# Kernel tuning notes

Hardware: AMD Instinct MI355X
Metric: run time of the kernel (lower is better)

Reference implementation:

```python
import jax, jax.numpy as jnp
import numpy as np

D_MODEL = 1024
N_HEADS = 16
D_HEAD = 64  # = d_model // num_heads = d_inner
LN_EPS = 1e-5


def setup_inputs() -> dict:
    key = jax.random.key(0)
    ks = jax.random.split(key, 8)
    B, CUR, PREV = 2, 1024, 1024
    T = CUR + PREV
    s = 0.02
    return {
        "x": jax.random.normal(ks[0], (B, CUR, D_MODEL), jnp.float32),
        "pos_emb": jax.random.normal(ks[1], (T, D_MODEL), jnp.float32),
        "u": jax.random.normal(ks[2], (N_HEADS, D_HEAD), jnp.float32),
        "v": jax.random.normal(ks[3], (N_HEADS, D_HEAD), jnp.float32),
        "tgt_mask": jnp.ones((B, CUR, T, 1), jnp.bool_),
        "mem": jax.random.normal(ks[4], (B, PREV, D_MODEL), jnp.float32),
        "Wq": jax.random.normal(ks[5], (D_MODEL, D_MODEL), jnp.float32) * s,
        "Wkv": jax.random.normal(ks[6], (2 * D_MODEL, D_MODEL), jnp.float32) * s,
        "Wfc": jax.random.normal(ks[7], (D_MODEL, D_MODEL), jnp.float32) * s,
        "bfc": jnp.zeros((D_MODEL,), jnp.float32),
        "gamma": jnp.ones((D_MODEL,), jnp.float32),
        "beta": jnp.zeros((D_MODEL,), jnp.float32),
    }


def _rel_shift(x):
    # Faithful port of the torch _rel_shift: pad along the query axis (dim=1),
    # reinterpret the contiguous buffer as (I+1, B, J, H), drop first row, reshape back.
    B, I, J, H = x.shape
    zero_pad = jnp.zeros((B, 1, J, H), x.dtype)
    x_padded = jnp.concatenate([zero_pad, x], axis=1).reshape(I + 1, B, J, H)
    return x_padded[1:].reshape(B, I, J, H)


def reference(x, pos_emb, u, v, tgt_mask, mem, Wq, Wkv, Wfc, bfc, gamma, beta):
    B, CUR, _ = x.shape
    h = jnp.concatenate([mem, x], axis=1)          # (B, T, d_model)
    T = h.shape[1]
    q = (x @ Wq.T).reshape(B, CUR, N_HEADS, D_HEAD)
    kv = h @ Wkv.T                                  # (B, T, 2*d_model)
    k, vv = jnp.split(kv, 2, axis=-1)
    k = k.reshape(B, T, N_HEADS, D_HEAD)
    vv = vv.reshape(B, T, N_HEADS, D_HEAD)

    content_attn = jnp.einsum('bihd,bjhd->bijh', q + u, k)
    pe = pos_emb.reshape(T, N_HEADS, D_HEAD)
    pos_attn = _rel_shift(jnp.einsum('bihd,jhd->bijh', q + v, pe))

    attn = content_attn + pos_attn                  # (B, I, J, H)
    attn = jnp.where(tgt_mask == 0, -jnp.inf, attn)  # mask BEFORE scaling (as original)
    attn = attn / (D_HEAD ** 0.5)
    attn = jax.nn.softmax(attn, axis=1)             # NOTE: original softmaxes over dim=1 (query axis)

    weighted = jnp.einsum('bijh,bjhd->bihd', attn, vv).reshape(B, CUR, -1)
    y = x + weighted @ Wfc.T + bfc                  # residual + fc (post-norm path)
    mu = jnp.mean(y, axis=-1, keepdims=True)
    var = jnp.var(y, axis=-1, keepdims=True)
    return (y - mu) / jnp.sqrt(var + LN_EPS) * gamma + beta
```

## Files before the change

### kernel.cpp

```cpp
#include <hip/hip_runtime.h>

#define DM   1024
#define CUR  1024
#define TT   2048

typedef float  f32x4  __attribute__((ext_vector_type(4)));
typedef __bf16 bf16_t;
typedef __bf16 bf16x8 __attribute__((ext_vector_type(8)));
typedef __bf16 bf16x4 __attribute__((ext_vector_type(4)));
typedef short  s16x4  __attribute__((ext_vector_type(4)));

#define SCALE_A 0.18033688f

static __device__ __forceinline__ float exp2fast(float x) { return __builtin_amdgcn_exp2f(x); }

static __device__ __forceinline__ f32x4 mfma32(bf16x8 a, bf16x8 b, f32x4 c) {
  return __builtin_amdgcn_mfma_f32_16x16x32_bf16(a, b, c, 0, 0, 0);
}
static __device__ __forceinline__ f32x4 mfma16(bf16x4 a, bf16x4 b, f32x4 c) {
  return __builtin_amdgcn_mfma_f32_16x16x16bf16_1k(
      __builtin_bit_cast(s16x4, a), __builtin_bit_cast(s16x4, b), c, 0, 0, 0);
}
static __device__ __forceinline__ void gl_lds16(const bf16_t* g, bf16_t* l) {
  __builtin_amdgcn_global_load_lds(
      (const __attribute__((address_space(1))) void*)g,
      (__attribute__((address_space(3))) void*)l, 16, 0, 0);
}

__global__ __launch_bounds__(256) void prep_kernel(const float* __restrict__ Wq,
                                                   const float* __restrict__ Wkv,
                                                   const float* __restrict__ Wfc,
                                                   const float* __restrict__ mem,
                                                   const float* __restrict__ x,
                                                   const float* __restrict__ pos,
                                                   bf16_t* __restrict__ wqb,
                                                   bf16_t* __restrict__ wkvb,
                                                   bf16_t* __restrict__ wfcb,
                                                   bf16_t* __restrict__ hb,
                                                   bf16_t* __restrict__ Bs) {
  int t = blockIdx.x * 256 + threadIdx.x;
  if (t < (1 << 20)) {
    const float* src; bf16_t* dst; int off;
    if (t < 262144)      { src = Wq;  dst = wqb;  off = t; }
    else if (t < 786432) { src = Wkv; dst = wkvb; off = t - 262144; }
    else                 { src = Wfc; dst = wfcb; off = t - 786432; }
    f32x4 v = *(const f32x4*)(src + (size_t)off * 4);
    bf16x4 o;
    o[0] = (bf16_t)v[0]; o[1] = (bf16_t)v[1]; o[2] = (bf16_t)v[2]; o[3] = (bf16_t)v[3];
    *(bf16x4*)(dst + (size_t)off * 4) = o;
  } else if (t < (2 << 20)) {
    int th = t - (1 << 20);
    int idx = th << 2;
    int b   = idx >> 21;
    int rem = idx & ((1 << 21) - 1);
    int tt  = rem >> 10;
    int c   = rem & 1023;
    const float* s = (tt < 1024)
        ? (mem + ((size_t)b * 1024 + tt) * DM + c)
        : (x   + ((size_t)b * 1024 + (tt - 1024)) * DM + c);
    f32x4 v = *(const f32x4*)s;
    bf16x4 o;
    o[0] = (bf16_t)v[0]; o[1] = (bf16_t)v[1]; o[2] = (bf16_t)v[2]; o[3] = (bf16_t)v[3];
    *(bf16x4*)(hb + idx) = o;
  } else {
    int tp = t - (2 << 20);
    int d4 = (tp & 15) << 2;
    int j  = (tp >> 4) & 2047;
    int bh = tp >> 15;
    int h  = bh & 15;
    f32x4 v = *(const f32x4*)(pos + (size_t)j * DM + h * 64 + d4);
    bf16x4 o;
    o[0] = (bf16_t)v[0]; o[1] = (bf16_t)v[1]; o[2] = (bf16_t)v[2]; o[3] = (bf16_t)v[3];
    *(bf16x4*)(Bs + ((size_t)bh * TT + j) * 128 + 64 + d4) = o;
  }
}

template<int WM>
__device__ __forceinline__ void gemm_core(const bf16_t* __restrict__ A,
                                          const bf16_t* __restrict__ B,
                                          int r0, int c0,
                                          bf16_t* At, bf16_t* Bt,
                                          f32x4 (&acc)[WM][4]) {
  const int ASZ = WM * 1024;
  const int BSZ = 4096;
  const int tid = threadIdx.x, w = tid >> 6, l = tid & 63;
  const int lm = l & 15, q = l >> 4;
  const int wrow = w >> 1, wcol = w & 1;
  const int gg  = (l & 3) ^ ((l >> 3) & 3);
  const int rsw = (lm >> 1) & 3;
  const bf16_t* gA = A + (size_t)(r0 + w * (WM / 2) * 16 + (l >> 2)) * 1024 + gg * 8;
  const bf16_t* gB = B + (size_t)(c0 + w * 32 + (l >> 2)) * 1024 + gg * 8;
  bf16_t* lA = At + w * (WM / 2) * 512;
  bf16_t* lB = Bt + w * 1024;
  const bf16_t* fA = At + (wrow * WM * 16 + lm) * 32;
  const bf16_t* fB = Bt + (wcol * 64 + lm) * 32;
#pragma unroll
  for (int t2 = 0; t2 < WM / 2; ++t2) gl_lds16(gA + (size_t)t2 * 16384, lA + t2 * 512);
#pragma unroll
  for (int t2 = 0; t2 < 2; ++t2)      gl_lds16(gB + (size_t)t2 * 16384, lB + t2 * 512);
  __syncthreads();
  int p = 0;
  for (int k0 = 0; k0 < 1024; k0 += 32) {
    int pn = p ^ 1;
    if (k0 < 992) {
#pragma unroll
      for (int t2 = 0; t2 < WM / 2; ++t2)
        gl_lds16(gA + (size_t)t2 * 16384 + k0 + 32, lA + pn * ASZ + t2 * 512);
#pragma unroll
      for (int t2 = 0; t2 < 2; ++t2)
        gl_lds16(gB + (size_t)t2 * 16384 + k0 + 32, lB + pn * BSZ + t2 * 512);
    }
    bf16x8 af[WM], bfm[4];
#pragma unroll
    for (int it = 0; it < WM; ++it)
      af[it] = *(const bf16x8*)(fA + p * ASZ + it * 512 + ((q ^ rsw) << 3));
#pragma unroll
    for (int jt = 0; jt < 4; ++jt)
      bfm[jt] = *(const bf16x8*)(fB + p * BSZ + jt * 512 + ((q ^ rsw) << 3));
#pragma unroll
    for (int it = 0; it < WM; ++it)
#pragma unroll
      for (int jt = 0; jt < 4; ++jt)
        acc[it][jt] = mfma32(af[it], bfm[jt], acc[it][jt]);
    __syncthreads();
    p = pn;
  }
}

__global__ __launch_bounds__(256) void k1_q(const bf16_t* __restrict__ hb,
                                            const bf16_t* __restrict__ Wqb,
                                            const float* __restrict__ u,
                                            const float* __restrict__ v,
                                            bf16_t* __restrict__ As) {
  __shared__ union { struct { bf16_t At[4096]; bf16_t Bt[8192]; } m; float Tt[4][272]; } sm;
  int blk = blockIdx.x;
  int r0 = (blk >> 3) * 64, c0 = (blk & 7) * 128;
  int b = r0 >> 10;
  const bf16_t* Axv = hb + ((size_t)(b + 1) << 20);
  f32x4 acc[2][4] = {};
  gemm_core<2>(Axv, Wqb, r0, c0, sm.m.At, sm.m.Bt, acc);
  const int tid = threadIdx.x, w = tid >> 6, l = tid & 63;
  const int lm = l & 15, q = l >> 4;
  const int wrow = w >> 1, wcol = w & 1;
  float* Tw = sm.Tt[w];
  int h = (c0 + wcol * 64) >> 6;
#pragma unroll
  for (int it = 0; it < 2; ++it) {
#pragma unroll
    for (int jt = 0; jt < 4; ++jt) {
#pragma unroll
      for (int r = 0; r < 4; ++r) Tw[(q * 4 + r) * 17 + lm] = acc[it][jt][r];
      __builtin_amdgcn_wave_barrier();
      int row = r0 + wrow * 32 + it * 16 + lm;
      int ii = row & 1023;
      int cbase = c0 + wcol * 64 + jt * 16 + q * 4;
      int d0 = cbase & 63;
      f32x4 u4 = *(const f32x4*)(u + cbase);
      f32x4 v4 = *(const f32x4*)(v + cbase);
      f32x4 tv;
#pragma unroll
      for (int e = 0; e < 4; ++e) tv[e] = Tw[lm * 17 + q * 4 + e];
      bf16x4 oc, op;
#pragma unroll
      for (int e = 0; e < 4; ++e) {
        oc[e] = (bf16_t)((tv[e] + u4[e]) * SCALE_A);
        op[e] = (bf16_t)((tv[e] + v4[e]) * SCALE_A);
      }
      *(bf16x4*)(As + (((size_t)(b * 16 + h)) * CUR + ii) * 128 + d0) = oc;
      if (b == 0) {
        if (ii >= 1)
          *(bf16x4*)(As + (((size_t)h) * CUR + (ii - 1)) * 128 + 64 + d0) = op;
        if (ii == 1023) {
          bf16x4 z = {};
          *(bf16x4*)(As + (((size_t)h) * CUR + 1023) * 128 + 64 + d0) = z;
        }
      } else {
        *(bf16x4*)(As + (((size_t)(16 + h)) * CUR + ii) * 128 + 64 + d0) = op;
      }
      __builtin_amdgcn_wave_barrier();
    }
  }
}

__global__ __launch_bounds__(256) void k2_kv(const bf16_t* __restrict__ hb,
                                             const bf16_t* __restrict__ Wkvb,
                                             bf16_t* __restrict__ Bs,
                                             bf16_t* __restrict__ vvT) {
  __shared__ union { struct { bf16_t At[8192]; bf16_t Bt[8192]; } m; float Tt[4][272]; } sm;
  int blk = blockIdx.x;
  int xcd = blk & 7, t = blk >> 3;
  int r0 = (t & 31) * 128;
  int c0 = (xcd * 2 + (t >> 5)) * 128;
  f32x4 acc[4][4] = {};
  gemm_core<4>(hb, Wkvb, r0, c0, sm.m.At, sm.m.Bt, acc);
  const int tid = threadIdx.x, w = tid >> 6, l = tid & 63;
  const int lm = l & 15, q = l >> 4;
  const int wrow = w >> 1, wcol = w & 1;
  int b = r0 >> 11;
  if (c0 < 1024) {
    float* Tw = sm.Tt[w];
    int h = (c0 + wcol * 64) >> 6;
#pragma unroll
    for (int it = 0; it < 4; ++it) {
#pragma unroll
      for (int jt = 0; jt < 4; ++jt) {
#pragma unroll
        for (int r = 0; r < 4; ++r) Tw[(q * 4 + r) * 17 + lm] = acc[it][jt][r];
        __builtin_amdgcn_wave_barrier();
        int j = (r0 + wrow * 64 + it * 16 + lm) & 2047;
        int d0 = jt * 16 + q * 4;
        bf16x4 o;
#pragma unroll
        for (int e = 0; e < 4; ++e) o[e] = (bf16_t)Tw[lm * 17 + q * 4 + e];
        *(bf16x4*)(Bs + (((size_t)(b * 16 + h)) * TT + j) * 128 + d0) = o;
        __builtin_amdgcn_wave_barrier();
      }
    }
  } else {
#pragma unroll
    for (int it = 0; it < 4; ++it) {
#pragma unroll
      for (int jt = 0; jt < 4; ++jt) {
        int c2 = c0 + wcol * 64 + jt * 16 + lm - 1024;
        int h = c2 >> 6, d = c2 & 63;
        int j = (r0 + wrow * 64 + it * 16 + q * 4) & 2047;
        bf16x4 o;
#pragma unroll
        for (int r = 0; r < 4; ++r) o[r] = (bf16_t)acc[it][jt][r];
        *(bf16x4*)(vvT + (((size_t)(b * 16 + h)) * 64 + d) * TT + j) = o;
      }
    }
  }
}

__global__ __launch_bounds__(256) void k3_stats(const bf16_t* __restrict__ As,
                                                const bf16_t* __restrict__ Bs,
                                                float* __restrict__ Lp) {
  __shared__ bf16_t At[2 * 8192];
  const int tid = threadIdx.x, w = tid >> 6, l = tid & 63;
  const int lm = l & 15, q = l >> 4;
  const int gg  = (l & 3) ^ ((l >> 3) & 3);
  const int rsw = (lm >> 1) & 3;
  int blk = blockIdx.x;
  int xcd = blk & 7, t = blk >> 3;
  int jblk = t & 7, ich = (t >> 3) & 3, bh = xcd * 4 + (t >> 5);
  int j0 = jblk * 256 + w * 64;
  const bf16_t* bsrow = Bs + ((size_t)bh * TT + j0 + lm) * 128 + q * 8;
  bf16x8 bfr[4][4];
#pragma unroll
  for (int js = 0; js < 4; ++js)
#pragma unroll
    for (int kt = 0; kt < 4; ++kt)
      bfr[js][kt] = *(const bf16x8*)(bsrow + js * 2048 + kt * 32);
  const bf16_t* abase = As + (size_t)bh * CUR * 128 +
                        (size_t)(ich * 256 + (l >> 2)) * 128 + w * 32 + gg * 8;
  bf16_t* lA = At + w * 2048;
  const bf16_t* fA = At + lm * 32;
  float lacc[4] = {0.f, 0.f, 0.f, 0.f};
#pragma unroll
  for (int t2 = 0; t2 < 4; ++t2)
    gl_lds16(abase + (size_t)t2 * 16 * 128, lA + t2 * 512);
  __syncthreads();
  int p = 0;
  for (int ib = 0; ib < 4; ++ib) {
    int pn = p ^ 1;
    if (ib < 3) {
#pragma unroll
      for (int t2 = 0; t2 < 4; ++t2)
        gl_lds16(abase + (size_t)((ib + 1) * 64 + t2 * 16) * 128, lA + pn * 8192 + t2 * 512);
    }
#pragma unroll
    for (int isub = 0; isub < 4; ++isub) {
      bf16x8 af[4];
#pragma unroll
      for (int kt = 0; kt < 4; ++kt)
        af[kt] = *(const bf16x8*)(fA + p * 8192 + kt * 2048 + isub * 512 + ((q ^ rsw) << 3));
      f32x4 s[4] = {};
#pragma unroll
      for (int js = 0; js < 4; ++js)
#pragma unroll
        for (int kt = 0; kt < 4; ++kt)
          s[js] = mfma32(af[kt], bfr[js][kt], s[js]);
#pragma unroll
      for (int js = 0; js < 4; ++js)
        lacc[js] += (exp2fast(s[js][0]) + exp2fast(s[js][1])) +
                    (exp2fast(s[js][2]) + exp2fast(s[js][3]));
    }
    __syncthreads();
    p = pn;
  }
#pragma unroll
  for (int js = 0; js < 4; ++js) {
#pragma unroll
    for (int off = 16; off <= 32; off <<= 1)
      lacc[js] += __shfl_xor(lacc[js], off, 64);
  }
  if (l < 16) {
    float* lp = Lp + (size_t)ich * 65536 + (size_t)bh * TT + j0;
#pragma unroll
    for (int js = 0; js < 4; ++js) lp[js * 16 + l] = lacc[js];
  }
}

__global__ __launch_bounds__(256) void vscale(const float* __restrict__ Lp,
                                              bf16_t* __restrict__ vvT) {
  int bh = blockIdx.x >> 3, jc = blockIdx.x & 7;
  int tid = threadIdx.x;
  int jj = jc * 256 + (tid & 63) * 4;
  int dg = tid >> 6;
  const float* lp = Lp + (size_t)bh * TT + jj;
  f32x4 a0 = *(const f32x4*)lp;
  f32x4 a1 = *(const f32x4*)(lp + 65536);
  f32x4 a2 = *(const f32x4*)(lp + 131072);
  f32x4 a3 = *(const f32x4*)(lp + 196608);
  f32x4 rl;
#pragma unroll
  for (int e = 0; e < 4; ++e)
    rl[e] = __builtin_amdgcn_rcpf((a0[e] + a1[e]) + (a2[e] + a3[e]));
  bf16_t* vb = vvT + ((size_t)bh * 64 + dg * 16) * TT + jj;
#pragma unroll
  for (int dd = 0; dd < 16; ++dd) {
    bf16x4 vv = *(const bf16x4*)(vb + (size_t)dd * TT);
    bf16x4 o;
#pragma unroll
    for (int e = 0; e < 4; ++e) o[e] = (bf16_t)((float)vv[e] * rl[e]);
    *(bf16x4*)(vb + (size_t)dd * TT) = o;
  }
}

__global__ __launch_bounds__(256, 2) void k4_attnv(const bf16_t* __restrict__ As,
                                                   const bf16_t* __restrict__ Bs,
                                                   const bf16_t* __restrict__ vvT,
                                                   bf16_t* __restrict__ Pp) {
  __shared__ union {
    struct { bf16_t Bt[2 * 8192]; bf16_t Vt[2 * 4096]; } m;
    float Tt[4][1088];
  } sm;
  int blk = blockIdx.x;
  int xcd = blk & 7, tb = blk >> 3;
  int iblk = tb & 3, pl = tb >> 2;
  int bh = xcd * 4 + (pl >> 3), jch = pl & 7;
  int b = bh >> 4, h = bh & 15;
  int i0 = iblk * 256;
  int jbase = jch * 256;
  const int tid = threadIdx.x, w = tid >> 6, l = tid & 63;
  const int lm = l & 15, q = l >> 4;
  const int gg  = (l & 3) ^ ((l >> 3) & 3);
  const int rsw = (lm >> 1) & 3;
  const bf16_t* ar = As + (size_t)bh * CUR * 128 + (size_t)(i0 + w * 64 + lm) * 128 + q * 8;
  bf16x8 bi[4][4];
#pragma unroll
  for (int is = 0; is < 4; ++is)
#pragma unroll
    for (int kt = 0; kt < 4; ++kt)
      bi[is][kt] = *(const bf16x8*)(ar + is * 2048 + kt * 32);
  const bf16_t* bbase = Bs + ((size_t)bh * TT + jbase) * 128 + (size_t)(l >> 2) * 128 + w * 32 + gg * 8;
  int inst0 = w * 2, inst1 = w * 2 + 1;
  const bf16_t* vsrc0 = vvT + ((size_t)bh * 64 + (inst0 & 3) * 16 + (l >> 2)) * TT + jbase +
                        (inst0 >> 2) * 32 + gg * 8;
  const bf16_t* vsrc1 = vvT + ((size_t)bh * 64 + (inst1 & 3) * 16 + (l >> 2)) * TT + jbase +
                        (inst1 >> 2) * 32 + gg * 8;
  bf16_t* vdst0 = sm.m.Vt + (inst0 >> 2) * 2048 + (inst0 & 3) * 512;
  bf16_t* vdst1 = sm.m.Vt + (inst1 >> 2) * 2048 + (inst1 & 3) * 512;
  bf16_t* lB = sm.m.Bt + w * 2048;
  f32x4 acc[4][4] = {};
#pragma unroll
  for (int t2 = 0; t2 < 4; ++t2)
    gl_lds16(bbase + (size_t)t2 * 16 * 128, lB + t2 * 512);
  gl_lds16(vsrc0, vdst0);
  gl_lds16(vsrc1, vdst1);
  __syncthreads();
  int p = 0;
  for (int jb = 0; jb < 4; ++jb) {
    int pn = p ^ 1;
    if (jb < 3) {
      const bf16_t* bs2 = bbase + (size_t)(jb + 1) * 64 * 128;
#pragma unroll
      for (int t2 = 0; t2 < 4; ++t2)
        gl_lds16(bs2 + (size_t)t2 * 16 * 128, lB + pn * 8192 + t2 * 512);
      gl_lds16(vsrc0 + (jb + 1) * 64, vdst0 + pn * 4096);
      gl_lds16(vsrc1 + (jb + 1) * 64, vdst1 + pn * 4096);
    }
    const bf16_t* fB = sm.m.Bt + p * 8192 + lm * 32;
    const bf16_t* vf = sm.m.Vt + p * 4096 + lm * 32;
#pragma unroll
    for (int js = 0; js < 4; ++js) {
      bf16x8 af[4];
#pragma unroll
      for (int kt = 0; kt < 4; ++kt)
        af[kt] = *(const bf16x8*)(fB + kt * 2048 + js * 512 + ((q ^ rsw) << 3));
      f32x4 s[4] = {};
#pragma unroll
      for (int is = 0; is < 4; ++is)
#pragma unroll
        for (int kt = 0; kt < 4; ++kt)
          s[is] = mfma32(af[kt], bi[is][kt], s[is]);
      bf16x4 pp[4];
#pragma unroll
      for (int is = 0; is < 4; ++is)
#pragma unroll
        for (int e = 0; e < 4; ++e)
          pp[is][e] = (bf16_t)exp2fast(s[is][e]);
      int vg = ((js & 1) << 1) | (q >> 1);
      const bf16_t* vfa = vf + (js >> 1) * 2048 + ((vg ^ rsw) << 3) + ((q & 1) << 2);
#pragma unroll
      for (int dt = 0; dt < 4; ++dt) {
        bf16x4 a2 = *(const bf16x4*)(vfa + dt * 512);
#pragma unroll
        for (int is = 0; is < 4; ++is)
          acc[is][dt] = mfma16(a2, pp[is], acc[is][dt]);
      }
    }
    __syncthreads();
    p = pn;
  }
  float* Tw = sm.Tt[w];
  bf16_t* pout = Pp + ((size_t)jch << 21);
  int ir = l >> 2, dc = (l & 3) * 16;
#pragma unroll
  for (int is = 0; is < 4; ++is) {
#pragma unroll
    for (int dt = 0; dt < 4; ++dt) {
      f32x4 a = acc[is][dt];
#pragma unroll
      for (int r = 0; r < 4; ++r) Tw[(dt * 16 + q * 4 + r) * 17 + lm] = a[r];
    }
    __builtin_amdgcn_wave_barrier();
    int i = i0 + w * 64 + is * 16 + ir;
    bf16_t* orow = pout + ((size_t)(b * CUR + i)) * DM + h * 64 + dc;
#pragma unroll
    for (int e4 = 0; e4 < 4; ++e4) {
      bf16x4 o;
#pragma unroll
      for (int e = 0; e < 4; ++e) o[e] = (bf16_t)Tw[(dc + e4 * 4 + e) * 17 + ir];
      *(bf16x4*)(orow + e4 * 4) = o;
    }
    __builtin_amdgcn_wave_barrier();
  }
}

__global__ __launch_bounds__(256) void k4_reduce(const bf16_t* __restrict__ P,
                                                 bf16_t* __restrict__ wbuf) {
  int t = blockIdx.x * 256 + threadIdx.x;
  float s[4] = {0.f, 0.f, 0.f, 0.f};
#pragma unroll
  for (int c = 0; c < 8; ++c) {
    bf16x4 v = *(const bf16x4*)(P + ((size_t)c << 21) + (size_t)t * 4);
#pragma unroll
    for (int e = 0; e < 4; ++e) s[e] += (float)v[e];
  }
  bf16x4 o;
#pragma unroll
  for (int e = 0; e < 4; ++e) o[e] = (bf16_t)s[e];
  *(bf16x4*)(wbuf + (size_t)t * 4) = o;
}

__global__ __launch_bounds__(256) void k5_fc(const bf16_t* __restrict__ wb,
                                             const bf16_t* __restrict__ Wfcb,
                                             const float* __restrict__ x,
                                             const float* __restrict__ bfc,
                                             float* __restrict__ y) {
  __shared__ union { struct { bf16_t At[4096]; bf16_t Bt[8192]; } m; float Tt[4][272]; } sm;
  int blk = blockIdx.x;
  int r0 = (blk >> 3) * 64, c0 = (blk & 7) * 128;
  f32x4 acc[2][4] = {};
  gemm_core<2>(wb, Wfcb, r0, c0, sm.m.At, sm.m.Bt, acc);
  const int tid = threadIdx.x, w = tid >> 6, l = tid & 63;
  const int lm = l & 15, q = l >> 4;
  const int wrow = w >> 1, wcol = w & 1;
  float* Tw = sm.Tt[w];
#pragma unroll
  for (int it = 0; it < 2; ++it) {
#pragma unroll
    for (int jt = 0; jt < 4; ++jt) {
#pragma unroll
      for (int r = 0; r < 4; ++r) Tw[(q * 4 + r) * 17 + lm] = acc[it][jt][r];
      __builtin_amdgcn_wave_barrier();
      int row = r0 + wrow * 32 + it * 16 + lm;
      int cb = c0 + wcol * 64 + jt * 16 + q * 4;
      f32x4 xb4 = *(const f32x4*)(x + (size_t)row * DM + cb);
      f32x4 bf4 = *(const f32x4*)(bfc + cb);
      f32x4 o;
#pragma unroll
      for (int e = 0; e < 4; ++e) o[e] = Tw[lm * 17 + q * 4 + e] + xb4[e] + bf4[e];
      *(f32x4*)(y + (size_t)row * DM + cb) = o;
      __builtin_amdgcn_wave_barrier();
    }
  }
}

__global__ __launch_bounds__(256) void k6_ln(const float* __restrict__ y,
                                             const float* __restrict__ gamma,
                                             const float* __restrict__ beta,
                                             float* __restrict__ out) {
  int row = blockIdx.x, t = threadIdx.x;
  const float* yr = y + (size_t)row * DM;
  f32x4 v = *(const f32x4*)(yr + t * 4);
  float s = v[0] + v[1] + v[2] + v[3];
  float ss = v[0] * v[0] + v[1] * v[1] + v[2] * v[2] + v[3] * v[3];
#pragma unroll
  for (int off = 1; off < 64; off <<= 1) {
    s += __shfl_xor(s, off, 64);
    ss += __shfl_xor(ss, off, 64);
  }
  __shared__ float ps[4], pss[4];
  int wv = t >> 6, ln = t & 63;
  if (ln == 0) { ps[wv] = s; pss[wv] = ss; }
  __syncthreads();
  s = ps[0] + ps[1] + ps[2] + ps[3];
  ss = pss[0] + pss[1] + pss[2] + pss[3];
  float mu = s * (1.0f / DM);
  float var = ss * (1.0f / DM) - mu * mu;
  float rstd = rsqrtf(var + 1e-5f);
  f32x4 g = *(const f32x4*)(gamma + t * 4);
  f32x4 bb = *(const f32x4*)(beta + t * 4);
  f32x4 o;
#pragma unroll
  for (int e = 0; e < 4; ++e) o[e] = (v[e] - mu) * rstd * g[e] + bb[e];
  *(f32x4*)(out + (size_t)row * DM + t * 4) = o;
}

extern "C" void kernel_launch(void* const* d_in, const int* in_sizes, int n_in,
                              void* d_out, int out_size, void* d_ws, size_t ws_size,
                              hipStream_t stream) {
  const float* x    = (const float*)d_in[0];
  const float* pos  = (const float*)d_in[1];
  const float* u    = (const float*)d_in[2];
  const float* v    = (const float*)d_in[3];
  const float* mem  = (const float*)d_in[5];
  const float* Wq   = (const float*)d_in[6];
  const float* Wkv  = (const float*)d_in[7];
  const float* Wfc  = (const float*)d_in[8];
  const float* bfc  = (const float*)d_in[9];
  const float* gam  = (const float*)d_in[10];
  const float* bet  = (const float*)d_in[11];
  float* out = (float*)d_out;

  char* ws = (char*)d_ws;
  const size_t MB = 1ull << 20;
  bf16_t* hb   = (bf16_t*)(ws);
  bf16_t* wqb  = (bf16_t*)(ws + 8 * MB);
  bf16_t* wkvb = (bf16_t*)(ws + 10 * MB);
  bf16_t* As   = (bf16_t*)(ws + 14 * MB);
  bf16_t* Bs   = (bf16_t*)(ws + 22 * MB);
  bf16_t* vvT  = (bf16_t*)(ws + 38 * MB);
  bf16_t* wfcb = (bf16_t*)(ws + 46 * MB);
  float*  Lp   = (float*) (ws + 48 * MB);
  bf16_t* Pp   = (bf16_t*)(ws + 49 * MB);
  bf16_t* wbuf = (bf16_t*)(ws);
  float*  y    = (float*) (ws + 4 * MB);

  prep_kernel<<<12288, 256, 0, stream>>>(Wq, Wkv, Wfc, mem, x, pos,
                                         wqb, wkvb, wfcb, hb, Bs);
  k1_q<<<256, 256, 0, stream>>>(hb, wqb, u, v, As);
  k2_kv<<<512, 256, 0, stream>>>(hb, wkvb, Bs, vvT);

  k3_stats<<<1024, 256, 0, stream>>>(As, Bs, Lp);
  vscale<<<256, 256, 0, stream>>>(Lp, vvT);
  k4_attnv<<<1024, 256, 0, stream>>>(As, Bs, vvT, Pp);
  k4_reduce<<<2048, 256, 0, stream>>>(Pp, wbuf);

  k5_fc<<<256, 256, 0, stream>>>(wbuf, wfcb, x, bfc, y);
  k6_ln<<<2048, 256, 0, stream>>>(y, gam, bet, out);
}
```

Measured before the change: 240.1 us.

## Merge Q and KV projection GEMMs into one launch; widen stats kernel tiles

The separate Q-projection and KV-projection kernels become one kernel of 768 blocks that branches on block index, so both GEMMs share a single launch and can fill the GPU together. The stats kernel now gives each wave 128 key columns instead of 64, holding twice as many B fragments in registers and launching half as many blocks. The aim is to cut launch overhead and tail idle time, and to reuse each LDS A-tile across more MFMAs. The costs are higher register pressure in the stats kernel, which may reduce occupancy, and a larger shared-memory allocation for the merged kernel's Q blocks.

```diff
diff --git a/kernel.cpp b/kernel.cpp
--- a/kernel.cpp
+++ b/kernel.cpp
@@ -127,107 +127,103 @@
   }
 }
 
-__global__ __launch_bounds__(256) void k1_q(const bf16_t* __restrict__ hb,
-                                            const bf16_t* __restrict__ Wqb,
-                                            const float* __restrict__ u,
-                                            const float* __restrict__ v,
-                                            bf16_t* __restrict__ As) {
-  __shared__ union { struct { bf16_t At[4096]; bf16_t Bt[8192]; } m; float Tt[4][272]; } sm;
-  int blk = blockIdx.x;
-  int r0 = (blk >> 3) * 64, c0 = (blk & 7) * 128;
-  int b = r0 >> 10;
-  const bf16_t* Axv = hb + ((size_t)(b + 1) << 20);
-  f32x4 acc[2][4] = {};
-  gemm_core<2>(Axv, Wqb, r0, c0, sm.m.At, sm.m.Bt, acc);
+__global__ __launch_bounds__(256) void k12_gemm(const bf16_t* __restrict__ hb,
+                                                const bf16_t* __restrict__ Wqb,
+                                                const bf16_t* __restrict__ Wkvb,
+                                                const float* __restrict__ u,
+                                                const float* __restrict__ v,
+                                                bf16_t* __restrict__ As,
+                                                bf16_t* __restrict__ Bs,
+                                                bf16_t* __restrict__ vvT) {
+  __shared__ union { struct { bf16_t At[8192]; bf16_t Bt[8192]; } m; float Tt[4][272]; } sm;
   const int tid = threadIdx.x, w = tid >> 6, l = tid & 63;
   const int lm = l & 15, q = l >> 4;
   const int wrow = w >> 1, wcol = w & 1;
-  float* Tw = sm.Tt[w];
-  int h = (c0 + wcol * 64) >> 6;
-#pragma unroll
-  for (int it = 0; it < 2; ++it) {
-#pragma unroll
-    for (int jt = 0; jt < 4; ++jt) {
-#pragma unroll
-      for (int r = 0; r < 4; ++r) Tw[(q * 4 + r) * 17 + lm] = acc[it][jt][r];
-      __builtin_amdgcn_wave_barrier();
-      int row = r0 + wrow * 32 + it * 16 + lm;
-      int ii = row & 1023;
-      int cbase = c0 + wcol * 64 + jt * 16 + q * 4;
-      int d0 = cbase & 63;
-      f32x4 u4 = *(const f32x4*)(u + cbase);
-      f32x4 v4 = *(const f32x4*)(v + cbase);
-      f32x4 tv;
-#pragma unroll
-      for (int e = 0; e < 4; ++e) tv[e] = Tw[lm * 17 + q * 4 + e];
-      bf16x4 oc, op;
-#pragma unroll
-      for (int e = 0; e < 4; ++e) {
-        oc[e] = (bf16_t)((tv[e] + u4[e]) * SCALE_A);
-        op[e] = (bf16_t)((tv[e] + v4[e]) * SCALE_A);
+  int blk = blockIdx.x;
+  if (blk < 512) {
+    int xcd = blk & 7, t = blk >> 3;
+    int r0 = (t & 31) * 128;
+    int c0 = (xcd * 2 + (t >> 5)) * 128;
+    f32x4 acc[4][4] = {};
+    gemm_core<4>(hb, Wkvb, r0, c0, sm.m.At, sm.m.Bt, acc);
+    int b = r0 >> 11;
+    if (c0 < 1024) {
+      float* Tw = sm.Tt[w];
+      int h = (c0 + wcol * 64) >> 6;
+#pragma unroll
+      for (int it = 0; it < 4; ++it) {
+#pragma unroll
+        for (int jt = 0; jt < 4; ++jt) {
+#pragma unroll
+          for (int r = 0; r < 4; ++r) Tw[(q * 4 + r) * 17 + lm] = acc[it][jt][r];
+          __builtin_amdgcn_wave_barrier();
+          int j = (r0 + wrow * 64 + it * 16 + lm) & 2047;
+          int d0 = jt * 16 + q * 4;
+          bf16x4 o;
+#pragma unroll
+          for (int e = 0; e < 4; ++e) o[e] = (bf16_t)Tw[lm * 17 + q * 4 + e];
+          *(bf16x4*)(Bs + (((size_t)(b * 16 + h)) * TT + j) * 128 + d0) = o;
+          __builtin_amdgcn_wave_barrier();
+        }
       }
-      *(bf16x4*)(As + (((size_t)(b * 16 + h)) * CUR + ii) * 128 + d0) = oc;
-      if (b == 0) {
-        if (ii >= 1)
-          *(bf16x4*)(As + (((size_t)h) * CUR + (ii - 1)) * 128 + 64 + d0) = op;
-        if (ii == 1023) {
-          bf16x4 z = {};
-          *(bf16x4*)(As + (((size_t)h) * CUR + 1023) * 128 + 64 + d0) = z;
+    } else {
+#pragma unroll
+      for (int it = 0; it < 4; ++it) {
+#pragma unroll
+        for (int jt = 0; jt < 4; ++jt) {
+          int c2 = c0 + wcol * 64 + jt * 16 + lm - 1024;
+          int h = c2 >> 6, d = c2 & 63;
+          int j = (r0 + wrow * 64 + it * 16 + q * 4) & 2047;
+          bf16x4 o;
+#pragma unroll
+          for (int r = 0; r < 4; ++r) o[r] = (bf16_t)acc[it][jt][r];
+          *(bf16x4*)(vvT + (((size_t)(b * 16 + h)) * 64 + d) * TT + j) = o;
         }
-      } else {
-        *(bf16x4*)(As + (((size_t)(16 + h)) * CUR + ii) * 128 + 64 + d0) = op;
       }
-      __builtin_amdgcn_wave_barrier();
-    }
-  }
-}
-
-__global__ __launch_bounds__(256) void k2_kv(const bf16_t* __restrict__ hb,
-                                             const bf16_t* __restrict__ Wkvb,
-                                             bf16_t* __restrict__ Bs,
-                                             bf16_t* __restrict__ vvT) {
-  __shared__ union { struct { bf16_t At[8192]; bf16_t Bt[8192]; } m; float Tt[4][272]; } sm;
-  int blk = blockIdx.x;
-  int xcd = blk & 7, t = blk >> 3;
-  int r0 = (t & 31) * 128;
-  int c0 = (xcd * 2 + (t >> 5)) * 128;
-  f32x4 acc[4][4] = {};
-  gemm_core<4>(hb, Wkvb, r0, c0, sm.m.At, sm.m.Bt, acc);
-  const int tid = threadIdx.x, w = tid >> 6, l = tid & 63;
-  const int lm = l & 15, q = l >> 4;
-  const int wrow = w >> 1, wcol = w & 1;
-  int b = r0 >> 11;
-  if (c0 < 1024) {
+    }
+  } else {
+    int blk2 = blk - 512;
+    int r0 = (blk2 >> 3) * 64, c0 = (blk2 & 7) * 128;
+    int b = r0 >> 10;
+    const bf16_t* Axv = hb + ((size_t)(b + 1) << 20);
+    f32x4 acc[2][4] = {};
+    gemm_core<2>(Axv, Wqb, r0, c0, sm.m.At, sm.m.Bt, acc);
     float* Tw = sm.Tt[w];
     int h = (c0 + wcol * 64) >> 6;
 #pragma unroll
-    for (int it = 0; it < 4; ++it) {
+    for (int it = 0; it < 2; ++it) {
 #pragma unroll
       for (int jt = 0; jt < 4; ++jt) {
 #pragma unroll
         for (int r = 0; r < 4; ++r) Tw[(q * 4 + r) * 17 + lm] = acc[it][jt][r];
         __builtin_amdgcn_wave_barrier();
-        int j = (r0 + wrow * 64 + it * 16 + lm) & 2047;
-        int d0 = jt * 16 + q * 4;
-        bf16x4 o;
-#pragma unroll
-        for (int e = 0; e < 4; ++e) o[e] = (bf16_t)Tw[lm * 17 + q * 4 + e];
-        *(bf16x4*)(Bs + (((size_t)(b * 16 + h)) * TT + j) * 128 + d0) = o;
+        int row = r0 + wrow * 32 + it * 16 + lm;
+        int ii = row & 1023;
+        int cbase = c0 + wcol * 64 + jt * 16 + q * 4;
+        int d0 = cbase & 63;
+        f32x4 u4 = *(const f32x4*)(u + cbase);
+        f32x4 v4 = *(const f32x4*)(v + cbase);
+        f32x4 tv;
+#pragma unroll
+        for (int e = 0; e < 4; ++e) tv[e] = Tw[lm * 17 + q * 4 + e];
+        bf16x4 oc, op;
+#pragma unroll
+        for (int e = 0; e < 4; ++e) {
+          oc[e] = (bf16_t)((tv[e] + u4[e]) * SCALE_A);
+          op[e] = (bf16_t)((tv[e] + v4[e]) * SCALE_A);
+        }
+        *(bf16x4*)(As + (((size_t)(b * 16 + h)) * CUR + ii) * 128 + d0) = oc;
+        if (b == 0) {
+          if (ii >= 1)
+            *(bf16x4*)(As + (((size_t)h) * CUR + (ii - 1)) * 128 + 64 + d0) = op;
+          if (ii == 1023) {
+            bf16x4 z = {};
+            *(bf16x4*)(As + (((size_t)h) * CUR + 1023) * 128 + 64 + d0) = z;
+          }
+        } else {
+          *(bf16x4*)(As + (((size_t)(16 + h)) * CUR + ii) * 128 + 64 + d0) = op;
+        }
         __builtin_amdgcn_wave_barrier();
-      }
-    }
-  } else {
-#pragma unroll
-    for (int it = 0; it < 4; ++it) {
-#pragma unroll
-      for (int jt = 0; jt < 4; ++jt) {
-        int c2 = c0 + wcol * 64 + jt * 16 + lm - 1024;
-        int h = c2 >> 6, d = c2 & 63;
-        int j = (r0 + wrow * 64 + it * 16 + q * 4) & 2047;
-        bf16x4 o;
-#pragma unroll
-        for (int r = 0; r < 4; ++r) o[r] = (bf16_t)acc[it][jt][r];
-        *(bf16x4*)(vvT + (((size_t)(b * 16 + h)) * 64 + d) * TT + j) = o;
       }
     }
   }
@@ -243,12 +239,12 @@
   const int rsw = (lm >> 1) & 3;
   int blk = blockIdx.x;
   int xcd = blk & 7, t = blk >> 3;
-  int jblk = t & 7, ich = (t >> 3) & 3, bh = xcd * 4 + (t >> 5);
-  int j0 = jblk * 256 + w * 64;
+  int jblk = t & 3, ich = (t >> 2) & 3, bh = xcd * 4 + (t >> 4);
+  int j0 = jblk * 512 + w * 128;
   const bf16_t* bsrow = Bs + ((size_t)bh * TT + j0 + lm) * 128 + q * 8;
-  bf16x8 bfr[4][4];
-#pragma unroll
-  for (int js = 0; js < 4; ++js)
+  bf16x8 bfr[8][4];
+#pragma unroll
+  for (int js = 0; js < 8; ++js)
 #pragma unroll
     for (int kt = 0; kt < 4; ++kt)
       bfr[js][kt] = *(const bf16x8*)(bsrow + js * 2048 + kt * 32);
@@ -256,7 +252,7 @@
                         (size_t)(ich * 256 + (l >> 2)) * 128 + w * 32 + gg * 8;
   bf16_t* lA = At + w * 2048;
   const bf16_t* fA = At + lm * 32;
-  float lacc[4] = {0.f, 0.f, 0.f, 0.f};
+  float lacc[8] = {};
 #pragma unroll
   for (int t2 = 0; t2 < 4; ++t2)
     gl_lds16(abase + (size_t)t2 * 16 * 128, lA + t2 * 512);
@@ -275,22 +271,20 @@
 #pragma unroll
       for (int kt = 0; kt < 4; ++kt)
         af[kt] = *(const bf16x8*)(fA + p * 8192 + kt * 2048 + isub * 512 + ((q ^ rsw) << 3));
-      f32x4 s[4] = {};
-#pragma unroll
-      for (int js = 0; js < 4; ++js)
+#pragma unroll
+      for (int js = 0; js < 8; ++js) {
+        f32x4 s = {};
 #pragma unroll
         for (int kt = 0; kt < 4; ++kt)
-          s[js] = mfma32(af[kt], bfr[js][kt], s[js]);
-#pragma unroll
-      for (int js = 0; js < 4; ++js)
-        lacc[js] += (exp2fast(s[js][0]) + exp2fast(s[js][1])) +
-                    (exp2fast(s[js][2]) + exp2fast(s[js][3]));
+          s = mfma32(af[kt], bfr[js][kt], s);
+        lacc[js] += (exp2fast(s[0]) + exp2fast(s[1])) + (exp2fast(s[2]) + exp2fast(s[3]));
+      }
     }
     __syncthreads();
     p = pn;
   }
 #pragma unroll
-  for (int js = 0; js < 4; ++js) {
+  for (int js = 0; js < 8; ++js) {
 #pragma unroll
     for (int off = 16; off <= 32; off <<= 1)
       lacc[js] += __shfl_xor(lacc[js], off, 64);
@@ -298,7 +292,7 @@
   if (l < 16) {
     float* lp = Lp + (size_t)ich * 65536 + (size_t)bh * TT + j0;
 #pragma unroll
-    for (int js = 0; js < 4; ++js) lp[js * 16 + l] = lacc[js];
+    for (int js = 0; js < 8; ++js) lp[js * 16 + l] = lacc[js];
   }
 }
 
@@ -552,10 +546,9 @@
 
   prep_kernel<<<12288, 256, 0, stream>>>(Wq, Wkv, Wfc, mem, x, pos,
                                          wqb, wkvb, wfcb, hb, Bs);
-  k1_q<<<256, 256, 0, stream>>>(hb, wqb, u, v, As);
-  k2_kv<<<512, 256, 0, stream>>>(hb, wkvb, Bs, vvT);
-
-  k3_stats<<<1024, 256, 0, stream>>>(As, Bs, Lp);
+  k12_gemm<<<768, 256, 0, stream>>>(hb, wqb, wkvb, u, v, As, Bs, vvT);
+
+  k3_stats<<<512, 256, 0, stream>>>(As, Bs, Lp);
   vscale<<<256, 256, 0, stream>>>(Lp, vvT);
   k4_attnv<<<1024, 256, 0, stream>>>(As, Bs, vvT, Pp);
   k4_reduce<<<2048, 256, 0, stream>>>(Pp, wbuf);
```

Measured after the change: 236.9 us (median of 2 runs). About the same (-1.3%).
